# Kernel tuning notes

Hardware: AMD Instinct MI355X
Metric: run time of the kernel (lower is better)

Reference implementation:

```python
import jax, jax.numpy as jnp
import numpy as np

ATTN_HEADS = 4
NEG = -1e9
LN_EPS = 1e-5


def _ln(x, s, b):
    m = x.mean(-1, keepdims=True)
    v = ((x - m) ** 2).mean(-1, keepdims=True)
    return (x - m) * jax.lax.rsqrt(v + LN_EPS) * s + b


def setup_inputs() -> dict:
    key = jax.random.key(0)
    ks = jax.random.split(key, 40)
    B, L, D, FF, NL = 512, 192, 256, 1024, 2
    V, U, I = 30000, 100000, 50000
    Lp, Ln, NF = 30, 300, 13
    Lu = jax.random.randint(ks[0], (B,), 1, L // 2)
    Li = jax.random.randint(ks[1], (B,), 1, L // 2)
    inp = {
        'attr': jax.random.randint(ks[2], (B, L), 0, V),
        'attr_inds': jax.random.randint(ks[3], (B, L), 0, 3),
        'attr_tf': jax.random.uniform(ks[4], (B, L), dtype=jnp.float32),
        'attr_feat': jax.random.normal(ks[5], (B, L, NF), dtype=jnp.float32),
        'attr_lens': Lu + Li,
        'attr_lens_user': Lu,
        'attr_lens_item': Li,
        'user_ids': jax.random.randint(ks[6], (B,), 0, U),
        'item_ids': jax.random.randint(ks[7], (B,), 0, I),
        'pos_targets': jax.random.randint(ks[8], (B, Lp), 0, V),
        'pos_lens': jax.random.randint(ks[9], (B,), 1, Lp + 1),
        'neg_targets': jax.random.randint(ks[10], (B, Ln), 0, V),
        'neg_lens': jax.random.randint(ks[11], (B,), 1, Ln + 1),
        # embedding tables (uniform(-0.1,0.1) per f_init_weight)
        'attr_emb': jax.random.uniform(ks[12], (V, D), minval=-0.1, maxval=0.1),
        'ind_emb': jax.random.uniform(ks[13], (3, D), minval=-0.1, maxval=0.1),
        'user_emb_table': jax.random.uniform(ks[14], (U, D), minval=-0.1, maxval=0.1),
        'item_emb_table': jax.random.uniform(ks[15], (I, D), minval=-0.1, maxval=0.1),
        'out_emb_user': jax.random.uniform(ks[16], (V, 2 * D), minval=-0.1, maxval=0.1),
        'out_emb_item': jax.random.uniform(ks[17], (V, 2 * D), minval=-0.1, maxval=0.1),
        # attr-weight head: Linear(13,1) + sigmoid
        'feat_w': jax.random.normal(ks[18], (NF,)) * 0.02,
        'feat_b': jnp.zeros(()),
        # transformer encoder params, stacked over NL layers
        'Wqkv': jax.random.normal(ks[19], (NL, 3 * D, D)) * 0.02,
        'bqkv': jnp.zeros((NL, 3 * D)),
        'Wo': jax.random.normal(ks[20], (NL, D, D)) * 0.02,
        'bo': jnp.zeros((NL, D)),
        'ln1_s': jnp.ones((NL, D)), 'ln1_b': jnp.zeros((NL, D)),
        'W1': jax.random.normal(ks[21], (NL, FF, D)) * 0.02,
        'b1': jnp.zeros((NL, FF)),
        'W2': jax.random.normal(ks[22], (NL, D, FF)) * 0.02,
        'b2': jnp.zeros((NL, D)),
        'ln2_s': jnp.ones((NL, D)), 'ln2_b': jnp.zeros((NL, D)),
    }
    return inp


def reference(attr, attr_inds, attr_tf, attr_feat, attr_lens, attr_lens_user,
              attr_lens_item, user_ids, item_ids, pos_targets, pos_lens,
              neg_targets, neg_lens, attr_emb, ind_emb, user_emb_table,
              item_emb_table, out_emb_user, out_emb_item, feat_w, feat_b,
              Wqkv, bqkv, Wo, bo, ln1_s, ln1_b, W1, b1, W2, b2, ln2_s, ln2_b):
    B, L = attr.shape
    D = attr_emb.shape[1]
    NL = Wqkv.shape[0]
    Dh = D // ATTN_HEADS
    pos = jnp.arange(L)
    valid = pos[None, :] < attr_lens[:, None]  # [B,L] True = valid key

    x = attr_emb[attr] + ind_emb[attr_inds]  # [B,L,D]
    for l in range(NL):  # post-LN TransformerEncoderLayer, relu, no dropout
        qkv = x @ Wqkv[l].T + bqkv[l]
        q, k, v = jnp.split(qkv, 3, axis=-1)
        q = q.reshape(B, L, ATTN_HEADS, Dh).transpose(0, 2, 1, 3)
        k = k.reshape(B, L, ATTN_HEADS, Dh).transpose(0, 2, 1, 3)
        v = v.reshape(B, L, ATTN_HEADS, Dh).transpose(0, 2, 1, 3)
        scores = jnp.einsum('bhqd,bhkd->bhqk', q, k) / np.sqrt(Dh).astype(x.dtype)
        scores = jnp.where(valid[:, None, None, :], scores, NEG)
        a = jax.nn.softmax(scores, axis=-1)
        ctx = jnp.einsum('bhqk,bhkd->bhqd', a, v).transpose(0, 2, 1, 3).reshape(B, L, D)
        x = _ln(x + ctx @ Wo[l].T + bo[l], ln1_s[l], ln1_b[l])
        ff = jax.nn.relu(x @ W1[l].T + b1[l]) @ W2[l].T + b2[l]
        x = _ln(x + ff, ln2_s[l], ln2_b[l])

    # ragged weighted segment average over user span [0,Lu) and item span [Lu,Lu+Li)
    w_user = jax.nn.sigmoid(attr_feat @ feat_w + feat_b)  # [B,L]
    wted = x * attr_tf[..., None]
    umask = pos[None, :] < attr_lens_user[:, None]
    imask = (~umask) & (pos[None, :] < (attr_lens_user + attr_lens_item)[:, None])
    user_x = (wted * w_user[..., None] * umask[..., None]).sum(1) / attr_lens_user[:, None].astype(x.dtype)
    item_x = (wted * (1.0 - w_user)[..., None] * imask[..., None]).sum(1) / attr_lens_item[:, None].astype(x.dtype)

    user_out = jnp.concatenate([user_x, user_emb_table[user_ids]], axis=-1)  # [B,2D]
    item_out = jnp.concatenate([item_x, item_emb_table[item_ids]], axis=-1)

    def logit(t):
        return (jnp.einsum('bkd,bd->bk', out_emb_user[t], user_out)
                + jnp.einsum('bkd,bd->bk', out_emb_item[t], item_out))

    pos_logits = logit(pos_targets)
    neg_logits = logit(neg_targets)
    pmask = jnp.arange(pos_targets.shape[1])[None, :] < pos_lens[:, None]
    nmask = jnp.arange(neg_targets.shape[1])[None, :] < neg_lens[:, None]
    logits = jnp.concatenate([pos_logits, neg_logits], axis=-1)
    mask = jnp.concatenate([pmask, nmask], axis=-1)
    new_targets = jnp.concatenate([jnp.ones_like(pos_targets), jnp.zeros_like(neg_targets)], axis=1) * mask
    return logits, mask, new_targets
```

## Files before the change

### kernel.cpp

```cpp
#include <hip/hip_runtime.h>
#include <hip/hip_bf16.h>
#include <cstdint>
#include <cstddef>

#define B_ 512
#define L_ 192
#define D_ 256
#define H_ 4
#define DH_ 64
#define FF_ 1024
#define NL_ 2
#define LP_ 30
#define LNEG_ 300
#define NF_ 13
#define M_ (B_*L_)
#define NT_ 330
#define V_ 30000

typedef __attribute__((ext_vector_type(8))) short bf16x8;
typedef __attribute__((ext_vector_type(4))) float f32x4;

__device__ __forceinline__ ushort f2b(float f) {
  union { float f; uint32_t u; } v; v.f = f;
  uint32_t u = v.u;
  return (ushort)((u + 0x7FFFu + ((u >> 16) & 1u)) >> 16);
}
__device__ __forceinline__ float b2f(ushort u) {
  union { uint32_t u; float f; } v; v.u = (uint32_t)u << 16; return v.f;
}

__global__ __launch_bounds__(512) void k_prefix(
    const int* __restrict__ lens, int* __restrict__ off,
    int* __restrict__ ccnt, int* __restrict__ ccntp, int Bc, int nchunks)
{
  const int t = threadIdx.x;
  int s = 0;
  for (int i = 0; i < t; ++i) s += lens[i];
  off[t] = s;
  if (t == 511) off[512] = s + lens[511];
  if (t < nchunks) {
    int s2 = 0;
    const int c0 = t * Bc;
    for (int i = 0; i < Bc; ++i) s2 += lens[c0 + i];
    ccnt[t]  = s2;
    ccntp[t] = (s2 + 127) & ~127;
  }
}

__global__ __launch_bounds__(256) void k_f2b(const float* __restrict__ in, ushort* __restrict__ out) {
  const int i = (blockIdx.x*256 + threadIdx.x)*8;
  float4 a = *(const float4*)(in+i);
  float4 b = *(const float4*)(in+i+4);
  ushort4 o1; o1.x=f2b(a.x); o1.y=f2b(a.y); o1.z=f2b(a.z); o1.w=f2b(a.w);
  ushort4 o2; o2.x=f2b(b.x); o2.y=f2b(b.y); o2.z=f2b(b.z); o2.w=f2b(b.w);
  *(ushort4*)(out+i)   = o1;
  *(ushort4*)(out+i+4) = o2;
}

__global__ __launch_bounds__(256) void k_f2b4(
    const float* __restrict__ wq, const float* __restrict__ wo,
    const float* __restrict__ w1, const float* __restrict__ w2,
    ushort* __restrict__ oq, ushort* __restrict__ oo,
    ushort* __restrict__ o1, ushort* __restrict__ o2)
{
  int bb = blockIdx.x;
  const float* in; ushort* out; int base;
  if (bb < 192)      { in = wq; out = oq; base = bb; }
  else if (bb < 256) { in = wo; out = oo; base = bb - 192; }
  else if (bb < 512) { in = w1; out = o1; base = bb - 256; }
  else               { in = w2; out = o2; base = bb - 512; }
  const int i = base*2048 + threadIdx.x*8;
  float4 a = *(const float4*)(in+i);
  float4 b = *(const float4*)(in+i+4);
  ushort4 q1; q1.x=f2b(a.x); q1.y=f2b(a.y); q1.z=f2b(a.z); q1.w=f2b(a.w);
  ushort4 q2; q2.x=f2b(b.x); q2.y=f2b(b.y); q2.z=f2b(b.z); q2.w=f2b(b.w);
  *(ushort4*)(out+i)   = q1;
  *(ushort4*)(out+i+4) = q2;
}

__global__ __launch_bounds__(256) void k_embed(
    const int* __restrict__ attr, const int* __restrict__ inds,
    const int* __restrict__ lens, const int* __restrict__ off,
    const float* __restrict__ attr_emb, const float* __restrict__ ind_emb,
    ushort* __restrict__ xb)
{
  int idx = blockIdx.x*256 + threadIdx.x;
  int token = idx >> 6;
  int c = (idx & 63) * 4;
  int b = token / L_;
  int l = token - b*L_;
  if (l >= lens[b]) return;
  size_t crow = (size_t)off[b] + l;
  int a = attr[token];
  int id = inds[token];
  const float4 e  = *(const float4*)(attr_emb + (size_t)a*D_ + c);
  const float4 ie = *(const float4*)(ind_emb  + (size_t)id*D_ + c);
  ushort4 ob; ob.x=f2b(e.x+ie.x); ob.y=f2b(e.y+ie.y); ob.z=f2b(e.z+ie.z); ob.w=f2b(e.w+ie.w);
  *(ushort4*)(xb + crow*D_ + c) = ob;
}

template<int OUT_BF16, int RELU>
__global__ __launch_bounds__(256) void k_gemm_mfma(
    const ushort* __restrict__ A, const int* __restrict__ aoffp,
    const int* __restrict__ cntp,
    const ushort* __restrict__ W, const float* __restrict__ bias,
    void* __restrict__ Cv, int N, int K)
{
  if ((int)blockIdx.y * 128 >= *cntp) return;
  __shared__ alignas(16) ushort As[8192];
  __shared__ alignas(16) ushort Bs[8192];
  const int abase = *aoffp;
  const int tid = threadIdx.x;
  const int w = tid >> 6, l = tid & 63;
  const int g = l >> 4, c16 = l & 15;
  const int m0 = blockIdx.y*128, n0 = blockIdx.x*128;
  const int wr = w >> 1, wc = w & 1;
  const int swzr = (c16 & 7) << 4;

  f32x4 acc[4][4];
  #pragma unroll
  for (int i=0;i<4;++i)
    #pragma unroll
    for (int j=0;j<4;++j) acc[i][j] = (f32x4){0.f,0.f,0.f,0.f};

  for (int k0=0; k0<K; k0+=64) {
    #pragma unroll
    for (int i=0;i<4;++i) {
      const int li  = i*4096 + tid*16;
      const int row = li >> 7;
      const int col = ((li & 127) ^ ((row & 7) << 4)) >> 1;
      const ushort* ga = A + (size_t)(abase+m0+row)*K + k0 + col;
      const ushort* gb = W + (size_t)(n0+row)*K + k0 + col;
      ushort* la = As + i*2048 + w*512;
      ushort* lb = Bs + i*2048 + w*512;
      __builtin_amdgcn_global_load_lds((const __attribute__((address_space(1))) unsigned int*)ga,
                                       (__attribute__((address_space(3))) unsigned int*)la, 16, 0, 0);
      __builtin_amdgcn_global_load_lds((const __attribute__((address_space(1))) unsigned int*)gb,
                                       (__attribute__((address_space(3))) unsigned int*)lb, 16, 0, 0);
    }
    __syncthreads();
    #pragma unroll
    for (int ks=0; ks<2; ++ks) {
      const int cb = ((g*16 + ks*64) ^ swzr) >> 1;
      bf16x8 af[4], bfr[4];
      #pragma unroll
      for (int i2=0;i2<4;++i2) {
        af[i2]  = *(const bf16x8*)(As + (size_t)(wr*64 + i2*16 + c16)*64 + cb);
        bfr[i2] = *(const bf16x8*)(Bs + (size_t)(wc*64 + i2*16 + c16)*64 + cb);
      }
      #pragma unroll
      for (int mi=0;mi<4;++mi)
        #pragma unroll
        for (int ni=0;ni<4;++ni)
          acc[mi][ni] = __builtin_amdgcn_mfma_f32_16x16x32_bf16(af[mi], bfr[ni], acc[mi][ni], 0,0,0);
    }
    __syncthreads();
  }
  const int col0 = n0 + wc*64 + c16;
  const int row0 = m0 + wr*64 + (g<<2);
  #pragma unroll
  for (int ni=0;ni<4;++ni) {
    const float bv = bias[col0 + ni*16];
    #pragma unroll
    for (int mi=0;mi<4;++mi) {
      #pragma unroll
      for (int r=0;r<4;++r) {
        float v = acc[mi][ni][r] + bv;
        if (RELU) v = fmaxf(v, 0.f);
        const size_t idx = (size_t)(row0 + mi*16 + r)*N + col0 + ni*16;
        if (OUT_BF16) ((ushort*)Cv)[idx] = f2b(v);
        else          ((float*)Cv)[idx]  = v;
      }
    }
  }
}

__global__ __launch_bounds__(512) void k_gemm_ln(
    const ushort* __restrict__ A,
    const int* __restrict__ cntp, const int* __restrict__ cnt,
    const int* __restrict__ xoffp,
    const ushort* __restrict__ W,
    const float* __restrict__ bias,
    const float* __restrict__ lns, const float* __restrict__ lnb,
    ushort* __restrict__ xb, int K)
{
  const int m0 = blockIdx.x*128;
  if (m0 >= *cntp) return;
  __shared__ alignas(16) ushort As[8192];
  __shared__ alignas(16) ushort Bs[16384];
  __shared__ float red[4][2][128];
  const int tid = threadIdx.x;
  const int w = tid >> 6, l = tid & 63;
  const int g = l >> 4, c16 = l & 15;
  const int wr = w >> 2, wc = w & 3;
  const int swzr = (c16 & 7) << 4;

  f32x4 acc[4][4];
  #pragma unroll
  for (int i=0;i<4;++i)
    #pragma unroll
    for (int j=0;j<4;++j) acc[i][j] = (f32x4){0.f,0.f,0.f,0.f};

  for (int k0=0; k0<K; k0+=64) {
    #pragma unroll
    for (int i=0;i<2;++i) {
      const int li  = i*8192 + tid*16;
      const int row = li >> 7;
      const int col = ((li & 127) ^ ((row & 7) << 4)) >> 1;
      const ushort* ga = A + (size_t)(m0+row)*K + k0 + col;
      ushort* la = As + i*4096 + w*512;
      __builtin_amdgcn_global_load_lds((const __attribute__((address_space(1))) unsigned int*)ga,
                                       (__attribute__((address_space(3))) unsigned int*)la, 16, 0, 0);
    }
    #pragma unroll
    for (int i=0;i<4;++i) {
      const int li  = i*8192 + tid*16;
      const int row = li >> 7;
      const int col = ((li & 127) ^ ((row & 7) << 4)) >> 1;
      const ushort* gb = W + (size_t)row*K + k0 + col;
      ushort* lb = Bs + i*4096 + w*512;
      __builtin_amdgcn_global_load_lds((const __attribute__((address_space(1))) unsigned int*)gb,
                                       (__attribute__((address_space(3))) unsigned int*)lb, 16, 0, 0);
    }
    __syncthreads();
    #pragma unroll
    for (int ks=0; ks<2; ++ks) {
      const int cb = ((g*16 + ks*64) ^ swzr) >> 1;
      bf16x8 af[4], bfr[4];
      #pragma unroll
      for (int i2=0;i2<4;++i2) {
        af[i2]  = *(const bf16x8*)(As + (size_t)(wr*64 + i2*16 + c16)*64 + cb);
        bfr[i2] = *(const bf16x8*)(Bs + (size_t)(wc*64 + i2*16 + c16)*64 + cb);
      }
      #pragma unroll
      for (int mi=0;mi<4;++mi)
        #pragma unroll
        for (int ni=0;ni<4;++ni)
          acc[mi][ni] = __builtin_amdgcn_mfma_f32_16x16x32_bf16(af[mi], bfr[ni], acc[mi][ni], 0,0,0);
    }
    __syncthreads();
  }

  const int xbase = *xoffp + m0;
  float bvs[4], svs[4], bbs[4];
  #pragma unroll
  for (int ni=0;ni<4;++ni) {
    int col = wc*64 + ni*16 + c16;
    bvs[ni] = bias[col]; svs[ni] = lns[col]; bbs[ni] = lnb[col];
  }
  float ps[4][4], pq[4][4];
  #pragma unroll
  for (int mi=0;mi<4;++mi) {
    #pragma unroll
    for (int r=0;r<4;++r) {
      ps[mi][r]=0.f; pq[mi][r]=0.f;
      const int lrow = wr*64 + mi*16 + 4*g + r;
      const ushort* xr = xb + (size_t)(xbase + lrow)*256;
      #pragma unroll
      for (int ni=0;ni<4;++ni) {
        float y = acc[mi][ni][r] + bvs[ni] + b2f(xr[wc*64 + ni*16 + c16]);
        acc[mi][ni][r] = y;
        ps[mi][r] += y;
        pq[mi][r] += y*y;
      }
    }
  }
  #pragma unroll
  for (int mi=0;mi<4;++mi)
    #pragma unroll
    for (int r=0;r<4;++r) {
      #pragma unroll
      for (int off=1; off<16; off<<=1) {
        ps[mi][r] += __shfl_xor(ps[mi][r], off, 16);
        pq[mi][r] += __shfl_xor(pq[mi][r], off, 16);
      }
    }
  if (c16 == 0) {
    #pragma unroll
    for (int mi=0;mi<4;++mi)
      #pragma unroll
      for (int r=0;r<4;++r) {
        const int lrow = wr*64 + mi*16 + 4*g + r;
        red[wc][0][lrow] = ps[mi][r];
        red[wc][1][lrow] = pq[mi][r];
      }
  }
  __syncthreads();
  const int cexact = *cnt;
  #pragma unroll
  for (int mi=0;mi<4;++mi) {
    #pragma unroll
    for (int r=0;r<4;++r) {
      const int lrow = wr*64 + mi*16 + 4*g + r;
      float tsum = red[0][0][lrow] + red[1][0][lrow] + red[2][0][lrow] + red[3][0][lrow];
      float tsq  = red[0][1][lrow] + red[1][1][lrow] + red[2][1][lrow] + red[3][1][lrow];
      float mean = tsum * (1.f/256.f);
      float var  = tsq * (1.f/256.f) - mean*mean;
      float inv  = rsqrtf(var + 1e-5f);
      if (m0 + lrow < cexact) {
        ushort* xbr = xb + (size_t)(xbase + lrow)*256;
        #pragma unroll
        for (int ni=0;ni<4;++ni) {
          int col = wc*64 + ni*16 + c16;
          xbr[col] = f2b((acc[mi][ni][r] - mean)*inv*svs[ni] + bbs[ni]);
        }
      }
    }
  }
}

__global__ __launch_bounds__(256) void k_attn_mfma(
    const ushort* __restrict__ qkv, ushort* __restrict__ ctx,
    const int* __restrict__ offc)
{
  __shared__ alignas(16) char lds[81920];
  char* Kb = lds;
  char* Vt = lds + 24576;
  const int tid = threadIdx.x;
  const int w = tid >> 6, l = tid & 63;
  const int g = l >> 4, c = l & 15;
  char* Pw = lds + 57344 + w*6144;
  const int bl = blockIdx.x >> 2, h = blockIdx.x & 3;
  const int rowbase = offc[bl] - offc[0];
  const int len = offc[bl+1] - offc[bl];
  const int nkt = (len + 15) >> 4;
  const int nkf = (len + 31) >> 5;
  const ushort* base = qkv + (size_t)rowbase*768;
  ushort* cbase = ctx + (size_t)rowbase*256;

  const int lenk8 = nkt*16*8;
  for (int idx = tid; idx < lenk8; idx += 256) {
    int row = idx >> 3, ch = idx & 7;
    uint4 v = *(const uint4*)(base + (size_t)row*768 + 256 + h*64 + ch*8);
    *(uint4*)(Kb + ((row*128 + ch*16) ^ ((row&7)<<4))) = v;
  }
  {
    const int lenv = nkf*32;
    int d0 = (tid & 15)*4;
    for (int key = tid >> 4; key < lenv; key += 16) {
      ushort4 v = *(const ushort4*)(base + (size_t)key*768 + 512 + h*64 + d0);
      ushort vv[4] = {v.x, v.y, v.z, v.w};
      #pragma unroll
      for (int j=0;j<4;++j) {
        int d = d0 + j;
        *(ushort*)(Vt + ((d*512 + key*2) ^ ((d&7)<<4))) = vv[j];
      }
    }
  }
  __syncthreads();

  for (int t = nkt; t < 2*nkf; ++t) {
    #pragma unroll
    for (int r=0;r<4;++r) {
      int q = 4*g + r;
      *(ushort*)(Pw + (((t>>1)*1024 + q*64 + ((t&1)*16 + c)*2) ^ (((q>>2)&3)<<4))) = 0;
    }
  }

  const int nst = (len + 15) >> 4;
  for (int s = w; s < nst; s += 4) {
    const ushort* qp = base + (size_t)(s*16 + c)*768 + h*64 + g*8;
    bf16x8 aq0 = *(const bf16x8*)qp;
    bf16x8 aq1 = *(const bf16x8*)(qp + 32);

    f32x4 sc[12];
    #pragma unroll
    for (int t=0;t<12;++t) {
      sc[t] = (f32x4){0.f,0.f,0.f,0.f};
      if (t < nkt) {
        int ba0 = ((t*16 + c)*128 + g*16)      ^ ((c&7)<<4);
        int ba1 = ((t*16 + c)*128 + g*16 + 64) ^ ((c&7)<<4);
        bf16x8 k0 = *(const bf16x8*)(Kb + ba0);
        bf16x8 k1 = *(const bf16x8*)(Kb + ba1);
        sc[t] = __builtin_amdgcn_mfma_f32_16x16x32_bf16(aq0, k0, sc[t], 0,0,0);
        sc[t] = __builtin_amdgcn_mfma_f32_16x16x32_bf16(aq1, k1, sc[t], 0,0,0);
        if (t == nkt-1 && t*16 + c >= len)
          sc[t] = (f32x4){-1e30f,-1e30f,-1e30f,-1e30f};
      }
    }
    float mr[4] = {-1e30f,-1e30f,-1e30f,-1e30f};
    #pragma unroll
    for (int t=0;t<12;++t) if (t<nkt) {
      #pragma unroll
      for (int r=0;r<4;++r) mr[r] = fmaxf(mr[r], sc[t][r]);
    }
    #pragma unroll
    for (int r=0;r<4;++r) {
      mr[r] = fmaxf(mr[r], __shfl_xor(mr[r], 1, 16));
      mr[r] = fmaxf(mr[r], __shfl_xor(mr[r], 2, 16));
      mr[r] = fmaxf(mr[r], __shfl_xor(mr[r], 4, 16));
      mr[r] = fmaxf(mr[r], __shfl_xor(mr[r], 8, 16));
    }
    float sr[4] = {0.f,0.f,0.f,0.f};
    #pragma unroll
    for (int t=0;t<12;++t) if (t<nkt) {
      #pragma unroll
      for (int r=0;r<4;++r) {
        float p = __expf((sc[t][r] - mr[r]) * 0.125f);
        sr[r] += p;
        int q = 4*g + r;
        *(ushort*)(Pw + (((t>>1)*1024 + q*64 + ((t&1)*16 + c)*2) ^ (((q>>2)&3)<<4))) = f2b(p);
      }
    }
    #pragma unroll
    for (int r=0;r<4;++r) {
      sr[r] += __shfl_xor(sr[r], 1, 16);
      sr[r] += __shfl_xor(sr[r], 2, 16);
      sr[r] += __shfl_xor(sr[r], 4, 16);
      sr[r] += __shfl_xor(sr[r], 8, 16);
    }
    f32x4 oa[4];
    #pragma unroll
    for (int dt=0;dt<4;++dt) oa[dt] = (f32x4){0.f,0.f,0.f,0.f};
    #pragma unroll
    for (int kf=0;kf<6;++kf) if (kf<nkf) {
      bf16x8 pf = *(const bf16x8*)(Pw + ((kf*1024 + c*64 + g*16) ^ (((c>>2)&3)<<4)));
      #pragma unroll
      for (int dt=0;dt<4;++dt) {
        int d = dt*16 + c;
        bf16x8 vf = *(const bf16x8*)(Vt + ((d*512 + kf*64 + g*16) ^ ((d&7)<<4)));
        oa[dt] = __builtin_amdgcn_mfma_f32_16x16x32_bf16(pf, vf, oa[dt], 0,0,0);
      }
    }
    float inv[4];
    #pragma unroll
    for (int r=0;r<4;++r) inv[r] = 1.f / sr[r];
    ushort* orow = cbase + (size_t)(s*16)*256 + h*64;
    #pragma unroll
    for (int r=0;r<4;++r) {
      int q = 4*g + r;
      if (s*16 + q < len) {
        #pragma unroll
        for (int dt=0;dt<4;++dt)
          orow[(size_t)q*256 + dt*16 + c] = f2b(oa[dt][r] * inv[r]);
      }
    }
  }
}

__global__ __launch_bounds__(256) void k_pool(
    const ushort* __restrict__ xb, const int* __restrict__ off,
    const float* __restrict__ attr_tf, const float* __restrict__ attr_feat,
    const int* __restrict__ lens_u, const int* __restrict__ lens_i,
    const int* __restrict__ user_ids, const int* __restrict__ item_ids,
    const float* __restrict__ user_tab, const float* __restrict__ item_tab,
    const float* __restrict__ feat_w, const float* __restrict__ feat_b,
    float* __restrict__ user_out, float* __restrict__ item_out)
{
  __shared__ float wu[L_], tf[L_];
  const int b = blockIdx.x;
  const int t = threadIdx.x;
  if (t < L_) {
    const float* f = attr_feat + ((size_t)b*L_ + t)*NF_;
    float sacc = feat_b[0];
    #pragma unroll
    for (int j=0;j<NF_;++j) sacc = fmaf(f[j], feat_w[j], sacc);
    wu[t] = 1.f/(1.f+__expf(-sacc));
    tf[t] = attr_tf[b*L_+t];
  }
  __syncthreads();
  const int Lu = lens_u[b], Li = lens_i[b];
  const ushort* xrow = xb + (size_t)off[b]*D_;
  float su=0.f, si=0.f;
  for (int l=0;l<Lu+Li;++l) {
    float val = b2f(xrow[(size_t)l*D_ + t]) * tf[l];
    if (l < Lu) su = fmaf(val, wu[l], su);
    else        si = fmaf(val, 1.f-wu[l], si);
  }
  user_out[(size_t)b*512 + t]       = su/(float)Lu;
  item_out[(size_t)b*512 + t]       = si/(float)Li;
  user_out[(size_t)b*512 + 256 + t] = user_tab[(size_t)user_ids[b]*D_ + t];
  item_out[(size_t)b*512 + 256 + t] = item_tab[(size_t)item_ids[b]*D_ + t];
}

__global__ __launch_bounds__(256) void k_logits(
    const int* __restrict__ pos_t, const int* __restrict__ neg_t,
    const int* __restrict__ pos_l, const int* __restrict__ neg_l,
    const ushort* __restrict__ oeu, const ushort* __restrict__ oei,
    const float* __restrict__ user_out, const float* __restrict__ item_out,
    float* __restrict__ out)
{
  const int g = blockIdx.x*4 + (threadIdx.x >> 6);
  const int lane = threadIdx.x & 63;
  const int b = g / NT_;
  const int k = g - b*NT_;
  const int tid_ = (k < LP_) ? pos_t[b*LP_ + k] : neg_t[b*LNEG_ + (k-LP_)];
  const ushort* eu = oeu + (size_t)tid_*512;
  const ushort* ei = oei + (size_t)tid_*512;
  const float* uo = user_out + (size_t)b*512;
  const float* io = item_out + (size_t)b*512;
  const int d0 = lane*8;
  float s = 0.f;
  ushort4 a0 = *(const ushort4*)(eu+d0), a1 = *(const ushort4*)(eu+d0+4);
  float4 u0 = *(const float4*)(uo+d0), u1 = *(const float4*)(uo+d0+4);
  s += b2f(a0.x)*u0.x + b2f(a0.y)*u0.y + b2f(a0.z)*u0.z + b2f(a0.w)*u0.w;
  s += b2f(a1.x)*u1.x + b2f(a1.y)*u1.y + b2f(a1.z)*u1.z + b2f(a1.w)*u1.w;
  ushort4 c0 = *(const ushort4*)(ei+d0), c1 = *(const ushort4*)(ei+d0+4);
  float4 i0 = *(const float4*)(io+d0), i1 = *(const float4*)(io+d0+4);
  s += b2f(c0.x)*i0.x + b2f(c0.y)*i0.y + b2f(c0.z)*i0.z + b2f(c0.w)*i0.w;
  s += b2f(c1.x)*i1.x + b2f(c1.y)*i1.y + b2f(c1.z)*i1.z + b2f(c1.w)*i1.w;
  #pragma unroll
  for (int off=32; off>0; off>>=1) s += __shfl_xor(s, off, 64);
  if (lane == 0) {
    out[(size_t)b*NT_ + k] = s;
    float mv, nt;
    if (k < LP_) { mv = (k < pos_l[b]) ? 1.f : 0.f; nt = mv; }
    else         { mv = ((k - LP_) < neg_l[b]) ? 1.f : 0.f; nt = 0.f; }
    out[(size_t)B_*NT_   + (size_t)b*NT_ + k] = mv;
    out[(size_t)2*B_*NT_ + (size_t)b*NT_ + k] = nt;
  }
}

extern "C" void kernel_launch(void* const* d_in, const int* in_sizes, int n_in,
                              void* d_out, int out_size, void* d_ws, size_t ws_size,
                              hipStream_t stream)
{
  const int*   attr      = (const int*)d_in[0];
  const int*   attr_inds = (const int*)d_in[1];
  const float* attr_tf   = (const float*)d_in[2];
  const float* attr_feat = (const float*)d_in[3];
  const int*   attr_lens = (const int*)d_in[4];
  const int*   lens_u    = (const int*)d_in[5];
  const int*   lens_i    = (const int*)d_in[6];
  const int*   user_ids  = (const int*)d_in[7];
  const int*   item_ids  = (const int*)d_in[8];
  const int*   pos_t     = (const int*)d_in[9];
  const int*   pos_l     = (const int*)d_in[10];
  const int*   neg_t     = (const int*)d_in[11];
  const int*   neg_l     = (const int*)d_in[12];
  const float* attr_emb  = (const float*)d_in[13];
  const float* ind_emb   = (const float*)d_in[14];
  const float* user_tab  = (const float*)d_in[15];
  const float* item_tab  = (const float*)d_in[16];
  const float* oeu       = (const float*)d_in[17];
  const float* oei       = (const float*)d_in[18];
  const float* feat_w    = (const float*)d_in[19];
  const float* feat_b    = (const float*)d_in[20];
  const float* Wqkv      = (const float*)d_in[21];
  const float* bqkv      = (const float*)d_in[22];
  const float* Wo        = (const float*)d_in[23];
  const float* bo        = (const float*)d_in[24];
  const float* ln1s      = (const float*)d_in[25];
  const float* ln1b      = (const float*)d_in[26];
  const float* W1        = (const float*)d_in[27];
  const float* b1        = (const float*)d_in[28];
  const float* W2        = (const float*)d_in[29];
  const float* b2        = (const float*)d_in[30];
  const float* ln2s      = (const float*)d_in[31];
  const float* ln2b      = (const float*)d_in[32];

  int* ioff  = (int*)d_ws;
  int* ccnt  = ioff + 520;
  int* ccntp = ccnt + 64;
  float* ws = (float*)d_ws + 768;
  float* uo = ws;
  float* io = uo + (size_t)B_*512;
  ushort* xb   = (ushort*)(io + (size_t)B_*512);
  ushort* wq_b = xb + (size_t)M_*D_;
  ushort* wo_b = wq_b + (size_t)2*768*256;
  ushort* w1_b = wo_b + (size_t)2*256*256;
  ushort* w2_b = w1_b + (size_t)2*1024*256;
  ushort* oeu_b = w2_b + (size_t)2*256*1024;
  ushort* oei_b = oeu_b + (size_t)V_*512;
  float* scratch = (float*)(oei_b + (size_t)V_*512);

  const size_t fixed_floats = 768 + (size_t)B_*1024 + (size_t)M_*(D_/2) + 786432 + (size_t)V_*512;
  int Bc = 8;
  for (int cand = 512; cand >= 8; cand >>= 1) {
    size_t need = (fixed_floats + (size_t)cand*L_*512) * sizeof(float);
    if (need <= ws_size) { Bc = cand; break; }
  }
  const int nchunks = B_ / Bc;
  const size_t Mc = (size_t)Bc * L_;

  float* out = (float*)d_out;

  k_prefix<<<1, 512, 0, stream>>>(attr_lens, ioff, ccnt, ccntp, Bc, nchunks);
  k_f2b4<<<768, 256, 0, stream>>>(Wqkv, Wo, W1, W2, wq_b, wo_b, w1_b, w2_b);
  k_f2b<<<(V_*512)/2048, 256, 0, stream>>>(oeu, oeu_b);
  k_f2b<<<(V_*512)/2048, 256, 0, stream>>>(oei, oei_b);
  k_embed<<<M_*64/256, 256, 0, stream>>>(attr, attr_inds, attr_lens, ioff, attr_emb, ind_emb, xb);

  for (int l=0; l<NL_; ++l) {
    const float* bqkv_l = bqkv + (size_t)l*768;
    const float* bo_l   = bo   + (size_t)l*D_;
    const float* b1_l   = b1   + (size_t)l*FF_;
    const float* b2_l   = b2   + (size_t)l*D_;
    for (int c=0; c<nchunks; ++c) {
      const int* offc = ioff + c*Bc;
      const int* cntp = ccntp + c;
      const int* cnt  = ccnt + c;
      ushort* qkv_b = (ushort*)scratch;
      ushort* ctx_b = (ushort*)(scratch + Mc*384);
      ushort* h_b   = (ushort*)scratch;

      k_gemm_mfma<1,0><<<dim3(768/128, Mc/128), 256, 0, stream>>>(
          xb, offc, cntp, wq_b + (size_t)l*768*256, bqkv_l, qkv_b, 768, 256);
      k_attn_mfma<<<Bc*H_, 256, 0, stream>>>(qkv_b, ctx_b, offc);
      k_gemm_ln<<<Mc/128, 512, 0, stream>>>(
          ctx_b, cntp, cnt, offc, wo_b + (size_t)l*256*256, bo_l,
          ln1s + (size_t)l*D_, ln1b + (size_t)l*D_, xb, 256);
      k_gemm_mfma<1,1><<<dim3(1024/128, Mc/128), 256, 0, stream>>>(
          xb, offc, cntp, w1_b + (size_t)l*1024*256, b1_l, h_b, 1024, 256);
      k_gemm_ln<<<Mc/128, 512, 0, stream>>>(
          h_b, cntp, cnt, offc, w2_b + (size_t)l*256*1024, b2_l,
          ln2s + (size_t)l*D_, ln2b + (size_t)l*D_, xb, 1024);
    }
  }
  k_pool<<<B_, 256, 0, stream>>>(xb, ioff, attr_tf, attr_feat, lens_u, lens_i, user_ids, item_ids,
                                 user_tab, item_tab, feat_w, feat_b, uo, io);
  k_logits<<<B_*NT_/4, 256, 0, stream>>>(pos_t, neg_t, pos_l, neg_l, oeu_b, oei_b, uo, io, out);
}
```

Measured before the change: 714.8 us.

## Fuse FFN up-projection, ReLU, down-projection and LayerNorm into one kernel

Replaces the separate W1 GEMM (which wrote the 1024-wide hidden activation to global scratch) and the W2 GEMM+LayerNorm kernel with a single kernel. Each block computes 128-column slices of the hidden layer in LDS and immediately accumulates them into the W2 output before applying bias, residual and LayerNorm. This removes the global write and read of the hidden tensor and one kernel launch per layer/chunk. In exchange, each block runs 512 threads with 64KB LDS, and grid parallelism is only Mc/128 blocks instead of the 8x-wider W1 grid. There is no double-buffering, so load latency may be exposed and occupancy may be lower.

Result: no change. 703.4 us (-1.6%).

```diff
diff --git a/kernel.cpp b/kernel.cpp
--- a/kernel.cpp
+++ b/kernel.cpp
@@ -303,6 +303,197 @@
         for (int ni=0;ni<4;++ni) {
           int col = wc*64 + ni*16 + c16;
           xbr[col] = f2b((acc[mi][ni][r] - mean)*inv*svs[ni] + bbs[ni]);
+        }
+      }
+    }
+  }
+}
+
+__global__ __launch_bounds__(512) void k_ffn(
+    const int* __restrict__ cntp, const int* __restrict__ cnt,
+    const int* __restrict__ xoffp,
+    const ushort* __restrict__ W1, const float* __restrict__ b1,
+    const ushort* __restrict__ W2, const float* __restrict__ b2,
+    const float* __restrict__ lns, const float* __restrict__ lnb,
+    ushort* __restrict__ xb)
+{
+  const int m0 = blockIdx.x*128;
+  if (m0 >= *cntp) return;
+  __shared__ alignas(16) char lds[65536];
+  __shared__ float red[4][2][128];
+  const int tid = threadIdx.x;
+  const int w = tid >> 6, l = tid & 63;
+  const int g = l >> 4, c16 = l & 15;
+  const int wr = w >> 2, wc = w & 3;
+  const int swzr = (c16 & 7) << 4;
+  const int xbase = *xoffp + m0;
+
+  f32x4 tac[4][4];
+  #pragma unroll
+  for (int i=0;i<4;++i)
+    #pragma unroll
+    for (int j=0;j<4;++j) tac[i][j] = (f32x4){0.f,0.f,0.f,0.f};
+
+  for (int s=0; s<8; ++s) {
+    f32x4 hac[4][2];
+    #pragma unroll
+    for (int i=0;i<4;++i)
+      #pragma unroll
+      for (int j=0;j<2;++j) hac[i][j] = (f32x4){0.f,0.f,0.f,0.f};
+    for (int kc=0; kc<4; ++kc) {
+      __syncthreads();
+      #pragma unroll
+      for (int i=0;i<2;++i) {
+        const int li  = i*8192 + tid*16;
+        const int row = li >> 7;
+        const int col = ((li & 127) ^ ((row & 7) << 4)) >> 1;
+        const ushort* ga = xb + (size_t)(xbase+row)*256 + kc*64 + col;
+        char* la = lds + i*8192 + w*1024;
+        __builtin_amdgcn_global_load_lds((const __attribute__((address_space(1))) unsigned int*)ga,
+                                         (__attribute__((address_space(3))) unsigned int*)la, 16, 0, 0);
+      }
+      #pragma unroll
+      for (int i=0;i<2;++i) {
+        const int li  = i*8192 + tid*16;
+        const int row = li >> 7;
+        const int col = ((li & 127) ^ ((row & 7) << 4)) >> 1;
+        const ushort* gb = W1 + (size_t)(s*128+row)*256 + kc*64 + col;
+        char* lb = lds + 16384 + i*8192 + w*1024;
+        __builtin_amdgcn_global_load_lds((const __attribute__((address_space(1))) unsigned int*)gb,
+                                         (__attribute__((address_space(3))) unsigned int*)lb, 16, 0, 0);
+      }
+      __syncthreads();
+      #pragma unroll
+      for (int ks=0; ks<2; ++ks) {
+        const int cb = (g*16 + ks*64) ^ swzr;
+        bf16x8 af[4], bf[2];
+        #pragma unroll
+        for (int mi=0;mi<4;++mi)
+          af[mi] = *(const bf16x8*)(lds + (wr*64 + mi*16 + c16)*128 + cb);
+        #pragma unroll
+        for (int ni=0;ni<2;++ni)
+          bf[ni] = *(const bf16x8*)(lds + 16384 + (wc*32 + ni*16 + c16)*128 + cb);
+        #pragma unroll
+        for (int mi=0;mi<4;++mi)
+          #pragma unroll
+          for (int ni=0;ni<2;++ni)
+            hac[mi][ni] = __builtin_amdgcn_mfma_f32_16x16x32_bf16(af[mi], bf[ni], hac[mi][ni], 0,0,0);
+      }
+    }
+    {
+      float bv1[2];
+      #pragma unroll
+      for (int ni=0;ni<2;++ni) bv1[ni] = b1[s*128 + wc*32 + ni*16 + c16];
+      #pragma unroll
+      for (int mi=0;mi<4;++mi)
+        #pragma unroll
+        for (int ni=0;ni<2;++ni)
+          #pragma unroll
+          for (int r=0;r<4;++r) {
+            int row = wr*64 + mi*16 + 4*g + r;
+            int colb = (wc*32 + ni*16 + c16)*2;
+            float h = fmaxf(hac[mi][ni][r] + bv1[ni], 0.f);
+            *(ushort*)(lds + 32768 + row*256 + (colb ^ ((row&7)<<4))) = f2b(h);
+          }
+    }
+    __syncthreads();
+    for (int kc2=0; kc2<2; ++kc2) {
+      if (kc2) __syncthreads();
+      #pragma unroll
+      for (int i=0;i<4;++i) {
+        const int li  = i*8192 + tid*16;
+        const int row = li >> 7;
+        const int col = ((li & 127) ^ ((row & 7) << 4)) >> 1;
+        const ushort* gb = W2 + (size_t)row*1024 + s*128 + kc2*64 + col;
+        char* lb = lds + i*8192 + w*1024;
+        __builtin_amdgcn_global_load_lds((const __attribute__((address_space(1))) unsigned int*)gb,
+                                         (__attribute__((address_space(3))) unsigned int*)lb, 16, 0, 0);
+      }
+      __syncthreads();
+      #pragma unroll
+      for (int ks=0; ks<2; ++ks) {
+        bf16x8 af[4], bf[4];
+        #pragma unroll
+        for (int mi=0;mi<4;++mi) {
+          int row = wr*64 + mi*16 + c16;
+          int colb = kc2*128 + g*16 + ks*64;
+          af[mi] = *(const bf16x8*)(lds + 32768 + row*256 + (colb ^ ((row&7)<<4)));
+        }
+        const int cb = (g*16 + ks*64) ^ swzr;
+        #pragma unroll
+        for (int ni=0;ni<4;++ni)
+          bf[ni] = *(const bf16x8*)(lds + (wc*64 + ni*16 + c16)*128 + cb);
+        #pragma unroll
+        for (int mi=0;mi<4;++mi)
+          #pragma unroll
+          for (int ni=0;ni<4;++ni)
+            tac[mi][ni] = __builtin_amdgcn_mfma_f32_16x16x32_bf16(af[mi], bf[ni], tac[mi][ni], 0,0,0);
+      }
+    }
+    __syncthreads();
+  }
+
+  float bvs[4], svs[4], bbs[4];
+  #pragma unroll
+  for (int ni=0;ni<4;++ni) {
+    int col = wc*64 + ni*16 + c16;
+    bvs[ni] = b2[col]; svs[ni] = lns[col]; bbs[ni] = lnb[col];
+  }
+  float ps[4][4], pq[4][4];
+  #pragma unroll
+  for (int mi=0;mi<4;++mi) {
+    #pragma unroll
+    for (int r=0;r<4;++r) {
+      ps[mi][r]=0.f; pq[mi][r]=0.f;
+      const int lrow = wr*64 + mi*16 + 4*g + r;
+      const ushort* xr = xb + (size_t)(xbase + lrow)*256;
+      #pragma unroll
+      for (int ni=0;ni<4;++ni) {
+        float y = tac[mi][ni][r] + bvs[ni] + b2f(xr[wc*64 + ni*16 + c16]);
+        tac[mi][ni][r] = y;
+        ps[mi][r] += y;
+        pq[mi][r] += y*y;
+      }
+    }
+  }
+  #pragma unroll
+  for (int mi=0;mi<4;++mi)
+    #pragma unroll
+    for (int r=0;r<4;++r) {
+      #pragma unroll
+      for (int off=1; off<16; off<<=1) {
+        ps[mi][r] += __shfl_xor(ps[mi][r], off, 16);
+        pq[mi][r] += __shfl_xor(pq[mi][r], off, 16);
+      }
+    }
+  if (c16 == 0) {
+    #pragma unroll
+    for (int mi=0;mi<4;++mi)
+      #pragma unroll
+      for (int r=0;r<4;++r) {
+        const int lrow = wr*64 + mi*16 + 4*g + r;
+        red[wc][0][lrow] = ps[mi][r];
+        red[wc][1][lrow] = pq[mi][r];
+      }
+  }
+  __syncthreads();
+  const int cexact = *cnt;
+  #pragma unroll
+  for (int mi=0;mi<4;++mi) {
+    #pragma unroll
+    for (int r=0;r<4;++r) {
+      const int lrow = wr*64 + mi*16 + 4*g + r;
+      float tsum = red[0][0][lrow] + red[1][0][lrow] + red[2][0][lrow] + red[3][0][lrow];
+      float tsq  = red[0][1][lrow] + red[1][1][lrow] + red[2][1][lrow] + red[3][1][lrow];
+      float mean = tsum * (1.f/256.f);
+      float var  = tsq * (1.f/256.f) - mean*mean;
+      float inv  = rsqrtf(var + 1e-5f);
+      if (m0 + lrow < cexact) {
+        ushort* xbr = xb + (size_t)(xbase + lrow)*256;
+        #pragma unroll
+        for (int ni=0;ni<4;++ni) {
+          int col = wc*64 + ni*16 + c16;
+          xbr[col] = f2b((tac[mi][ni][r] - mean)*inv*svs[ni] + bbs[ni]);
         }
       }
     }
@@ -592,7 +783,6 @@
       const int* cnt  = ccnt + c;
       ushort* qkv_b = (ushort*)scratch;
       ushort* ctx_b = (ushort*)(scratch + Mc*384);
-      ushort* h_b   = (ushort*)scratch;
 
       k_gemm_mfma<1,0><<<dim3(768/128, Mc/128), 256, 0, stream>>>(
           xb, offc, cntp, wq_b + (size_t)l*768*256, bqkv_l, qkv_b, 768, 256);
@@ -600,11 +790,10 @@
       k_gemm_ln<<<Mc/128, 512, 0, stream>>>(
           ctx_b, cntp, cnt, offc, wo_b + (size_t)l*256*256, bo_l,
           ln1s + (size_t)l*D_, ln1b + (size_t)l*D_, xb, 256);
-      k_gemm_mfma<1,1><<<dim3(1024/128, Mc/128), 256, 0, stream>>>(
-          xb, offc, cntp, w1_b + (size_t)l*1024*256, b1_l, h_b, 1024, 256);
-      k_gemm_ln<<<Mc/128, 512, 0, stream>>>(
-          h_b, cntp, cnt, offc, w2_b + (size_t)l*256*1024, b2_l,
-          ln2s + (size_t)l*D_, ln2b + (size_t)l*D_, xb, 1024);
+      k_ffn<<<Mc/128, 512, 0, stream>>>(
+          cntp, cnt, offc, w1_b + (size_t)l*1024*256, b1_l,
+          w2_b + (size_t)l*256*1024, b2_l,
+          ln2s + (size_t)l*D_, ln2b + (size_t)l*D_, xb);
     }
   }
   k_pool<<<B_, 256, 0, stream>>>(xb, ioff, attr_tf, attr_feat, lens_u, lens_i, user_ids, item_ids,
```
